# Kernel optimization log

Measured on AMD Instinct MI355X. Metric: run time of the kernel, lower is better.

Reference implementation:

```python
import jax, jax.numpy as jnp
import numpy as np

B, S, D, H = 4, 2048, 1024, 16
DK = D // H  # 64


def setup_inputs() -> dict:
    key = jax.random.key(0)
    ks = jax.random.split(key, 9)
    x = jax.random.normal(ks[0], (B, S, D), dtype=jnp.float32)
    # causal mask, broadcast over batch and heads
    attn_mask = jnp.tril(jnp.ones((S, S), dtype=jnp.int32))[None, None]
    scale = 0.02
    Wq = jax.random.normal(ks[1], (D, D), dtype=jnp.float32) * scale
    Wk = jax.random.normal(ks[2], (D, D), dtype=jnp.float32) * scale
    Wv = jax.random.normal(ks[3], (D, D), dtype=jnp.float32) * scale
    Wo = jax.random.normal(ks[4], (D, D), dtype=jnp.float32) * scale
    bq = jax.random.normal(ks[5], (D,), dtype=jnp.float32) * scale
    bk = jax.random.normal(ks[6], (D,), dtype=jnp.float32) * scale
    bv = jax.random.normal(ks[7], (D,), dtype=jnp.float32) * scale
    bo = jax.random.normal(ks[8], (D,), dtype=jnp.float32) * scale
    return {"x": x, "attn_mask": attn_mask, "Wq": Wq, "bq": bq, "Wk": Wk,
            "bk": bk, "Wv": Wv, "bv": bv, "Wo": Wo, "bo": bo}


def reference(x, attn_mask, Wq, bq, Wk, bk, Wv, bv, Wo, bo):
    b, s, d = x.shape
    # projections -> [b, h, s, dk]
    def proj(W, bias):
        return (x @ W + bias).reshape(b, s, H, DK).transpose(0, 2, 1, 3)
    q = proj(Wq, bq)
    k = proj(Wk, bk)
    v = proj(Wv, bv)
    # scores [b, h, s, s]
    scores = jnp.einsum('bhqd,bhkd->bhqk', q, k) / jnp.sqrt(jnp.float32(DK))
    scores = jnp.where(attn_mask == 0, jnp.float32(-1e9), scores)
    probs = jax.nn.softmax(scores, axis=-1)  # dropout_rate=0 -> identity
    attn_out = jnp.einsum('bhqk,bhkd->bhqd', probs, v)
    # combine heads -> [b, s, d], then output projection
    attn_out = attn_out.transpose(0, 2, 1, 3).reshape(b, s, d)
    return attn_out @ Wo + bo
```

## Files before the change

### kernel.cpp

```cpp
#include <hip/hip_runtime.h>
#include <hip/hip_bf16.h>
#include <stdint.h>

#define S_LEN 2048
#define DMODEL 1024
#define NH 16
#define DK 64
#define BATCH 4
#define KDIM 1024
#define SCQ 0.18033688f

using bf16 = __hip_bfloat16;
using bf162 = __hip_bfloat162;

typedef __bf16 v_bf16x8 __attribute__((ext_vector_type(8)));
typedef short v_s16x4 __attribute__((ext_vector_type(4)));
typedef float v_f32x4 __attribute__((ext_vector_type(4)));

union PackB4 { v_s16x4 v; bf162 h[2]; };

__device__ __forceinline__ void gll16(const void* g, void* l) {
    __builtin_amdgcn_global_load_lds(
        (__attribute__((address_space(1))) unsigned int*)g,
        (__attribute__((address_space(3))) unsigned int*)l, 16, 0, 0);
}

struct alignas(8) BF4 { bf16 a, b, c, d; };

__global__ __launch_bounds__(256) void prep(
    const float* __restrict__ x, bf16* __restrict__ xb,
    const float* __restrict__ W0, const float* __restrict__ W1,
    const float* __restrict__ W2, const float* __restrict__ W3,
    bf16* __restrict__ Wt4)
{
    const int z = blockIdx.z;
    const int t = threadIdx.x;
    if (z == 4) {
        int bid = blockIdx.y * 32 + blockIdx.x;
        size_t base4 = (size_t)bid * 2048 + t;
        #pragma unroll
        for (int j = 0; j < 8; j++) {
            size_t i4 = base4 + j * 256;
            float4 v = *(const float4*)(x + i4 * 4);
            BF4 r;
            r.a = __float2bfloat16(v.x);
            r.b = __float2bfloat16(v.y);
            r.c = __float2bfloat16(v.z);
            r.d = __float2bfloat16(v.w);
            *(BF4*)(xb + i4 * 4) = r;
        }
        return;
    }
    __shared__ float tile[32][33];
    const float* W = (z == 0) ? W0 : (z == 1) ? W1 : (z == 2) ? W2 : W3;
    bf16* Wt = Wt4 + (size_t)z * DMODEL * DMODEL;
    const float sc = (z == 0) ? SCQ : 1.0f;
    int tx = t & 31, ty = t >> 5;
    int k0 = blockIdx.x * 32, n0 = blockIdx.y * 32;
    #pragma unroll
    for (int i = 0; i < 4; i++) {
        int k = k0 + ty + 8 * i;
        tile[ty + 8 * i][tx] = W[(size_t)k * DMODEL + n0 + tx];
    }
    __syncthreads();
    #pragma unroll
    for (int i = 0; i < 4; i++) {
        int n = n0 + ty + 8 * i;
        Wt[(size_t)n * DMODEL + k0 + tx] = __float2bfloat16(tile[tx][ty + 8 * i] * sc);
    }
}

__global__ __launch_bounds__(256) void gemm_qkv(
    const bf16* __restrict__ A, const bf16* __restrict__ Wt4,
    const float* __restrict__ bq, const float* __restrict__ bk,
    const float* __restrict__ bv,
    bf16* __restrict__ Qo, bf16* __restrict__ Ko, bf16* __restrict__ Vto)
{
    __shared__ __align__(16) short lds[16384];
    const int z = blockIdx.z;
    const bf16* Bt = Wt4 + (size_t)z * DMODEL * DMODEL;
    const float* bias = (z == 0) ? bq : (z == 1) ? bk : bv;
    const float bsc = (z == 0) ? SCQ : 1.0f;

    const int t = threadIdx.x;
    const int lane = t & 63;
    const int wave = t >> 6;
    const int quad = lane >> 4;
    const int l15 = lane & 15;
    const int m0 = blockIdx.x * 128;
    const int n0 = blockIdx.y * 128;
    const int wRow = (wave >> 1) * 64;
    const int wCol = (wave & 1) * 64;

    const int r0 = t >> 2, p0 = t & 3;
    const int r1 = (t + 256) >> 2, p1 = (t + 256) & 3;

    const bf16* gA0 = A  + (size_t)(m0 + r0) * KDIM + p0 * 8;
    const bf16* gA1 = A  + (size_t)(m0 + r1) * KDIM + p1 * 8;
    const bf16* gB0 = Bt + (size_t)(n0 + r0) * KDIM + p0 * 8;
    const bf16* gB1 = Bt + (size_t)(n0 + r1) * KDIM + p1 * 8;

    v_f32x4 acc[4][4] = {};

    gll16(gA0, lds + t * 8);
    gll16(gA1, lds + t * 8 + 2048);
    gll16(gB0, lds + 4096 + t * 8);
    gll16(gB1, lds + 4096 + t * 8 + 2048);
    __syncthreads();

    int cur = 0;
    for (int k0 = 0; k0 < KDIM; k0 += 32) {
        if (k0 + 32 < KDIM) {
            short* Ad = lds + (cur ^ 1) * 8192;
            short* Bd = Ad + 4096;
            gll16(gA0 + k0 + 32, Ad + t * 8);
            gll16(gA1 + k0 + 32, Ad + t * 8 + 2048);
            gll16(gB0 + k0 + 32, Bd + t * 8);
            gll16(gB1 + k0 + 32, Bd + t * 8 + 2048);
        }
        const short* As = lds + cur * 8192;
        const short* Bs = As + 4096;
        const short* ArowBase = (z == 2) ? Bs : As;
        const short* BrowBase = (z == 2) ? As : Bs;

        v_bf16x8 af[4], bfr[4];
        #pragma unroll
        for (int mt = 0; mt < 4; mt++) {
            int r = wRow + mt * 16 + l15;
            af[mt] = *(const v_bf16x8*)(ArowBase + r * 32 + quad * 8);
        }
        #pragma unroll
        for (int nt = 0; nt < 4; nt++) {
            int r = wCol + nt * 16 + l15;
            bfr[nt] = *(const v_bf16x8*)(BrowBase + r * 32 + quad * 8);
        }
        __builtin_amdgcn_s_setprio(1);
        #pragma unroll
        for (int mt = 0; mt < 4; mt++)
            #pragma unroll
            for (int nt = 0; nt < 4; nt++)
                acc[mt][nt] = __builtin_amdgcn_mfma_f32_16x16x32_bf16(
                    af[mt], bfr[nt], acc[mt][nt], 0, 0, 0);
        __builtin_amdgcn_s_setprio(0);

        __syncthreads();
        cur ^= 1;
    }

    if (z != 2) {
        bf16* C = (z == 0) ? Qo : Ko;
        float bvv[4];
        #pragma unroll
        for (int nt = 0; nt < 4; nt++)
            bvv[nt] = bias[n0 + wCol + nt * 16 + l15] * bsc;
        #pragma unroll
        for (int mt = 0; mt < 4; mt++)
            #pragma unroll
            for (int nt = 0; nt < 4; nt++)
                #pragma unroll
                for (int r = 0; r < 4; r++) {
                    int row = m0 + wRow + mt * 16 + quad * 4 + r;
                    int col = n0 + wCol + nt * 16 + l15;
                    int b = row >> 11, s = row & (S_LEN - 1);
                    int h = col >> 6, dk = col & (DK - 1);
                    C[(((size_t)(b * NH + h)) * S_LEN + s) * DK + dk] =
                        __float2bfloat16(acc[mt][nt][r] + bvv[nt]);
                }
    } else {
        float bvv[4][4];
        #pragma unroll
        for (int mt = 0; mt < 4; mt++)
            #pragma unroll
            for (int r = 0; r < 4; r++)
                bvv[mt][r] = bias[n0 + wRow + mt * 16 + quad * 4 + r];
        #pragma unroll
        for (int mt = 0; mt < 4; mt++)
            #pragma unroll
            for (int nt = 0; nt < 4; nt++)
                #pragma unroll
                for (int r = 0; r < 4; r++) {
                    int ng = n0 + wRow + mt * 16 + quad * 4 + r;
                    int rowg = m0 + wCol + nt * 16 + l15;
                    int b = rowg >> 11, s = rowg & (S_LEN - 1);
                    int h = ng >> 6, dk = ng & (DK - 1);
                    Vto[(((size_t)(b * NH + h)) * DK + dk) * S_LEN + s] =
                        __float2bfloat16(acc[mt][nt][r] + bvv[mt][r]);
                }
    }
}

__global__ __launch_bounds__(256) void gemm_o(
    const bf16* __restrict__ A, const bf16* __restrict__ Bt,
    const float* __restrict__ bias, float* __restrict__ C)
{
    __shared__ __align__(16) short lds[16384];
    const int t = threadIdx.x;
    const int lane = t & 63;
    const int wave = t >> 6;
    const int quad = lane >> 4;
    const int l15 = lane & 15;
    const int m0 = blockIdx.x * 128;
    const int n0 = blockIdx.y * 128;
    const int wRow = (wave >> 1) * 64;
    const int wCol = (wave & 1) * 64;

    const int r0 = t >> 2, p0 = t & 3;
    const int r1 = (t + 256) >> 2, p1 = (t + 256) & 3;

    const bf16* gA0 = A  + (size_t)(m0 + r0) * KDIM + p0 * 8;
    const bf16* gA1 = A  + (size_t)(m0 + r1) * KDIM + p1 * 8;
    const bf16* gB0 = Bt + (size_t)(n0 + r0) * KDIM + p0 * 8;
    const bf16* gB1 = Bt + (size_t)(n0 + r1) * KDIM + p1 * 8;

    v_f32x4 acc[4][4] = {};

    gll16(gA0, lds + t * 8);
    gll16(gA1, lds + t * 8 + 2048);
    gll16(gB0, lds + 4096 + t * 8);
    gll16(gB1, lds + 4096 + t * 8 + 2048);
    __syncthreads();

    int cur = 0;
    for (int k0 = 0; k0 < KDIM; k0 += 32) {
        if (k0 + 32 < KDIM) {
            short* Ad = lds + (cur ^ 1) * 8192;
            short* Bd = Ad + 4096;
            gll16(gA0 + k0 + 32, Ad + t * 8);
            gll16(gA1 + k0 + 32, Ad + t * 8 + 2048);
            gll16(gB0 + k0 + 32, Bd + t * 8);
            gll16(gB1 + k0 + 32, Bd + t * 8 + 2048);
        }
        const short* As = lds + cur * 8192;
        const short* Bs = As + 4096;

        v_bf16x8 af[4], bfr[4];
        #pragma unroll
        for (int mt = 0; mt < 4; mt++) {
            int r = wRow + mt * 16 + l15;
            af[mt] = *(const v_bf16x8*)(As + r * 32 + quad * 8);
        }
        #pragma unroll
        for (int nt = 0; nt < 4; nt++) {
            int r = wCol + nt * 16 + l15;
            bfr[nt] = *(const v_bf16x8*)(Bs + r * 32 + quad * 8);
        }
        __builtin_amdgcn_s_setprio(1);
        #pragma unroll
        for (int mt = 0; mt < 4; mt++)
            #pragma unroll
            for (int nt = 0; nt < 4; nt++)
                acc[mt][nt] = __builtin_amdgcn_mfma_f32_16x16x32_bf16(
                    af[mt], bfr[nt], acc[mt][nt], 0, 0, 0);
        __builtin_amdgcn_s_setprio(0);

        __syncthreads();
        cur ^= 1;
    }

    float bvv[4];
    #pragma unroll
    for (int nt = 0; nt < 4; nt++) bvv[nt] = bias[n0 + wCol + nt * 16 + l15];

    #pragma unroll
    for (int mt = 0; mt < 4; mt++)
        #pragma unroll
        for (int nt = 0; nt < 4; nt++)
            #pragma unroll
            for (int r = 0; r < 4; r++) {
                int row = m0 + wRow + mt * 16 + quad * 4 + r;
                int col = n0 + wCol + nt * 16 + l15;
                C[(size_t)row * DMODEL + col] = acc[mt][nt][r] + bvv[nt];
            }
}

__global__ __launch_bounds__(256) void attn_mfma(
    const bf16* __restrict__ Qg, const bf16* __restrict__ Kg,
    const bf16* __restrict__ Vtg, bf16* __restrict__ Og)
{
    __shared__ __align__(16) short lds[16384];

    const int t = threadIdx.x;
    const int lane = t & 63;
    const int wave = t >> 6;
    const int quad = lane >> 4;
    const int l15 = lane & 15;
    const int bh = blockIdx.x;
    const int ybal[16] = {15, 8, 7, 0, 14, 9, 6, 1, 13, 10, 5, 2, 12, 11, 4, 3};
    const int by = blockIdx.y;
    const int yy = ybal[(by & 3) * 4 + (by >> 2)];
    const int q0 = yy * 128;
    const int ntiles = 2 * (yy + 1);

    const size_t baseK = (size_t)bh * S_LEN * DK;
    const size_t baseVt = (size_t)bh * DK * S_LEN;

    const int cr = t >> 3;
    const int cs = (t & 7) ^ (cr & 7);
    const bf16* srcK = Kg + baseK + (size_t)cr * DK + cs * 8;
    const bf16* srcV = Vtg + baseVt + (size_t)cr * S_LEN + cs * 8;

    v_bf16x8 qf[2][2];
    #pragma unroll
    for (int qt = 0; qt < 2; qt++) {
        int q = q0 + wave * 32 + qt * 16 + l15;
        #pragma unroll
        for (int kc = 0; kc < 2; kc++)
            qf[qt][kc] = *(const v_bf16x8*)(Qg + baseK + (size_t)q * DK + kc * 32 + quad * 8);
    }

    v_f32x4 oacc[2][4] = {};
    float lrun[2] = {0.f, 0.f};

    {
        short* Kd = lds;
        short* Vd = lds + 4096;
        gll16(srcK, Kd + t * 8);
        gll16(srcK + 32 * DK, Kd + t * 8 + 2048);
        gll16(srcV, Vd + t * 8);
        gll16(srcV + 32 * S_LEN, Vd + t * 8 + 2048);
    }
    __syncthreads();

    int cur = 0;
    for (int tt = 0; tt < ntiles; tt++) {
        if (tt + 1 < ntiles) {
            short* Kd = lds + (cur ^ 1) * 8192;
            short* Vd = Kd + 4096;
            const bf16* sk = srcK + (size_t)(tt + 1) * (64 * DK);
            const bf16* sv = srcV + (size_t)(tt + 1) * 64;
            gll16(sk, Kd + t * 8);
            gll16(sk + 32 * DK, Kd + t * 8 + 2048);
            gll16(sv, Vd + t * 8);
            gll16(sv + 32 * S_LEN, Vd + t * 8 + 2048);
        }
        const short* Ks = lds + cur * 8192;
        const short* Vs = Ks + 4096;

        v_f32x4 s_[4][2];
        __builtin_amdgcn_s_setprio(1);
        #pragma unroll
        for (int kt = 0; kt < 4; kt++) {
            int krow = kt * 16 + l15;
            v_bf16x8 kf0 = *(const v_bf16x8*)(Ks + krow * 64 + ((quad) ^ (krow & 7)) * 8);
            v_bf16x8 kf1 = *(const v_bf16x8*)(Ks + krow * 64 + ((4 + quad) ^ (krow & 7)) * 8);
            #pragma unroll
            for (int qt = 0; qt < 2; qt++) {
                v_f32x4 a = {};
                a = __builtin_amdgcn_mfma_f32_16x16x32_bf16(kf0, qf[qt][0], a, 0, 0, 0);
                a = __builtin_amdgcn_mfma_f32_16x16x32_bf16(kf1, qf[qt][1], a, 0, 0, 0);
                s_[kt][qt] = a;
            }
        }
        __builtin_amdgcn_s_setprio(0);

        if (tt >= ntiles - 2) {
            int kbase = (tt - (ntiles - 2)) * 64;
            #pragma unroll
            for (int kt = 0; kt < 4; kt++)
                #pragma unroll
                for (int qt = 0; qt < 2; qt++) {
                    int qq = wave * 32 + qt * 16 + l15;
                    #pragma unroll
                    for (int r = 0; r < 4; r++) {
                        int key = kbase + kt * 16 + quad * 4 + r;
                        if (key > qq) s_[kt][qt][r] = -1e30f;
                    }
                }
        }

        #pragma unroll
        for (int kt = 0; kt < 4; kt++)
            #pragma unroll
            for (int qt = 0; qt < 2; qt++) {
                float p0 = __builtin_amdgcn_exp2f(s_[kt][qt][0]);
                float p1 = __builtin_amdgcn_exp2f(s_[kt][qt][1]);
                float p2 = __builtin_amdgcn_exp2f(s_[kt][qt][2]);
                float p3 = __builtin_amdgcn_exp2f(s_[kt][qt][3]);
                s_[kt][qt][0] = p0; s_[kt][qt][1] = p1;
                s_[kt][qt][2] = p2; s_[kt][qt][3] = p3;
                lrun[qt] += (p0 + p1) + (p2 + p3);
            }

        __builtin_amdgcn_s_setprio(1);
        #pragma unroll
        for (int kt = 0; kt < 4; kt++) {
            v_s16x4 vf[4];
            #pragma unroll
            for (int dt = 0; dt < 4; dt++) {
                vf[dt] = *(const v_s16x4*)(Vs + (dt * 16 + l15) * 64 +
                                           ((kt * 2 + (quad >> 1)) ^ (l15 & 7)) * 8 +
                                           (quad & 1) * 4);
            }
            #pragma unroll
            for (int qt = 0; qt < 2; qt++) {
                PackB4 pu;
                pu.h[0] = __float22bfloat162_rn(make_float2(s_[kt][qt][0], s_[kt][qt][1]));
                pu.h[1] = __float22bfloat162_rn(make_float2(s_[kt][qt][2], s_[kt][qt][3]));
                #pragma unroll
                for (int dt = 0; dt < 4; dt++)
                    oacc[qt][dt] = __builtin_amdgcn_mfma_f32_16x16x16bf16_1k(
                        vf[dt], pu.v, oacc[qt][dt], 0, 0, 0);
            }
        }
        __builtin_amdgcn_s_setprio(0);

        __syncthreads();
        cur ^= 1;
    }

    #pragma unroll
    for (int qt = 0; qt < 2; qt++) {
        lrun[qt] += __shfl_xor(lrun[qt], 16);
        lrun[qt] += __shfl_xor(lrun[qt], 32);
    }
    #pragma unroll
    for (int qt = 0; qt < 2; qt++) {
        float inv = 1.f / lrun[qt];
        int qloc = wave * 32 + qt * 16 + l15;
        #pragma unroll
        for (int dt = 0; dt < 4; dt++) {
            PackB4 ou;
            ou.h[0] = __float22bfloat162_rn(
                make_float2(oacc[qt][dt][0] * inv, oacc[qt][dt][1] * inv));
            ou.h[1] = __float22bfloat162_rn(
                make_float2(oacc[qt][dt][2] * inv, oacc[qt][dt][3] * inv));
            *(v_s16x4*)(lds + qloc * 72 + dt * 16 + quad * 4) = ou.v;
        }
    }
    __syncthreads();
    {
        const int b = bh >> 4, h = bh & 15;
        int row = t >> 1, half = t & 1;
        size_t gbase = (((size_t)b * S_LEN + q0 + row) * NH + h) * DK + half * 32;
        #pragma unroll
        for (int j = 0; j < 4; j++)
            *(uint4*)(Og + gbase + j * 8) =
                *(const uint4*)(lds + row * 72 + half * 32 + j * 8);
    }
}

extern "C" void kernel_launch(void* const* d_in, const int* in_sizes, int n_in,
                              void* d_out, int out_size, void* d_ws, size_t ws_size,
                              hipStream_t stream) {
    const float* x  = (const float*)d_in[0];
    const float* Wq = (const float*)d_in[2];
    const float* bq = (const float*)d_in[3];
    const float* Wk = (const float*)d_in[4];
    const float* bk = (const float*)d_in[5];
    const float* Wv = (const float*)d_in[6];
    const float* bv = (const float*)d_in[7];
    const float* Wo = (const float*)d_in[8];
    const float* bo = (const float*)d_in[9];
    float* out = (float*)d_out;

    const size_t TEN = (size_t)BATCH * S_LEN * DMODEL * sizeof(bf16);
    char* ws = (char*)d_ws;
    bf16* xb  = (bf16*)ws;
    bf16* Vt  = (bf16*)(ws + TEN);
    bf16* Wt4 = (bf16*)(ws + 2 * TEN);
    bf16* Q   = (bf16*)d_out;
    bf16* Kt  = (bf16*)((char*)d_out + TEN);
    bf16* AO  = xb;

    hipLaunchKernelGGL(prep, dim3(32, 32, 5), dim3(256),
                       0, stream, x, xb, Wq, Wk, Wv, Wo, Wt4);

    hipLaunchKernelGGL(gemm_qkv, dim3(BATCH * S_LEN / 128, DMODEL / 128, 3), dim3(256),
                       0, stream, xb, Wt4, bq, bk, bv, Q, Kt, Vt);

    hipLaunchKernelGGL(attn_mfma, dim3(BATCH * NH, S_LEN / 128), dim3(256),
                       0, stream, Q, Kt, Vt, AO);

    hipLaunchKernelGGL(gemm_o, dim3(BATCH * S_LEN / 128, DMODEL / 128), dim3(256),
                       0, stream, AO, Wt4 + (size_t)3 * DMODEL * DMODEL, bo, out);
}
```

Measured before the change: 255.6 us.

## Replace syncthreads with explicit vmcnt waits and compute softmax row sums via MFMA

In both projection GEMMs, the full __syncthreads before and after each K step becomes an explicit s_waitcnt vmcnt on the async LDS loads plus a raw s_barrier, so the next tile's prefetch can stay in flight across the barrier. In the attention kernel, the per-row probability sums are now accumulated with an extra MFMA against a ones vector instead of scalar adds and cross-lane shuffles. The probabilities are packed to bf16 once and V-fragment LDS addresses are precomputed. This trades VALU and shuffle work for extra MFMA issue, and the denominator is now summed from bf16-rounded probabilities, matching the numerator's rounding.

```diff
diff --git a/kernel.cpp b/kernel.cpp
--- a/kernel.cpp
+++ b/kernel.cpp
@@ -106,7 +106,6 @@
     gll16(gA1, lds + t * 8 + 2048);
     gll16(gB0, lds + 4096 + t * 8);
     gll16(gB1, lds + 4096 + t * 8 + 2048);
-    __syncthreads();
 
     int cur = 0;
     for (int k0 = 0; k0 < KDIM; k0 += 32) {
@@ -117,7 +116,13 @@
             gll16(gA1 + k0 + 32, Ad + t * 8 + 2048);
             gll16(gB0 + k0 + 32, Bd + t * 8);
             gll16(gB1 + k0 + 32, Bd + t * 8 + 2048);
-        }
+            asm volatile("s_waitcnt vmcnt(4)" ::: "memory");
+        } else {
+            asm volatile("s_waitcnt vmcnt(0)" ::: "memory");
+        }
+        __builtin_amdgcn_sched_barrier(0);
+        __builtin_amdgcn_s_barrier();
+
         const short* As = lds + cur * 8192;
         const short* Bs = As + 4096;
         const short* ArowBase = (z == 2) ? Bs : As;
@@ -143,7 +148,9 @@
                     af[mt], bfr[nt], acc[mt][nt], 0, 0, 0);
         __builtin_amdgcn_s_setprio(0);
 
-        __syncthreads();
+        asm volatile("s_waitcnt lgkmcnt(0)" ::: "memory");
+        __builtin_amdgcn_sched_barrier(0);
+        __builtin_amdgcn_s_barrier();
         cur ^= 1;
     }
 
@@ -218,7 +225,6 @@
     gll16(gA1, lds + t * 8 + 2048);
     gll16(gB0, lds + 4096 + t * 8);
     gll16(gB1, lds + 4096 + t * 8 + 2048);
-    __syncthreads();
 
     int cur = 0;
     for (int k0 = 0; k0 < KDIM; k0 += 32) {
@@ -229,7 +235,13 @@
             gll16(gA1 + k0 + 32, Ad + t * 8 + 2048);
             gll16(gB0 + k0 + 32, Bd + t * 8);
             gll16(gB1 + k0 + 32, Bd + t * 8 + 2048);
-        }
+            asm volatile("s_waitcnt vmcnt(4)" ::: "memory");
+        } else {
+            asm volatile("s_waitcnt vmcnt(0)" ::: "memory");
+        }
+        __builtin_amdgcn_sched_barrier(0);
+        __builtin_amdgcn_s_barrier();
+
         const short* As = lds + cur * 8192;
         const short* Bs = As + 4096;
 
@@ -253,7 +265,9 @@
                     af[mt], bfr[nt], acc[mt][nt], 0, 0, 0);
         __builtin_amdgcn_s_setprio(0);
 
-        __syncthreads();
+        asm volatile("s_waitcnt lgkmcnt(0)" ::: "memory");
+        __builtin_amdgcn_sched_barrier(0);
+        __builtin_amdgcn_s_barrier();
         cur ^= 1;
     }
 
@@ -308,8 +322,19 @@
             qf[qt][kc] = *(const v_bf16x8*)(Qg + baseK + (size_t)q * DK + kc * 32 + quad * 8);
     }
 
+    int vfA[4][4];
+    #pragma unroll
+    for (int kt = 0; kt < 4; kt++)
+        #pragma unroll
+        for (int dt = 0; dt < 4; dt++)
+            vfA[kt][dt] = ((dt * 16 + l15) * 64 +
+                           ((kt * 2 + (quad >> 1)) ^ (l15 & 7)) * 8 +
+                           (quad & 1) * 4) * 2 + 8192;
+
+    const v_s16x4 ones = {(short)0x3F80, (short)0x3F80, (short)0x3F80, (short)0x3F80};
+
     v_f32x4 oacc[2][4] = {};
-    float lrun[2] = {0.f, 0.f};
+    v_f32x4 lacc[2] = {};
 
     {
         short* Kd = lds;
@@ -333,8 +358,8 @@
             gll16(sv, Vd + t * 8);
             gll16(sv + 32 * S_LEN, Vd + t * 8 + 2048);
         }
+        const int cb = cur << 14;
         const short* Ks = lds + cur * 8192;
-        const short* Vs = Ks + 4096;
 
         v_f32x4 s_[4][2];
         __builtin_amdgcn_s_setprio(1);
@@ -368,6 +393,7 @@
                 }
         }
 
+        PackB4 pk[4][2];
         #pragma unroll
         for (int kt = 0; kt < 4; kt++)
             #pragma unroll
@@ -376,9 +402,8 @@
                 float p1 = __builtin_amdgcn_exp2f(s_[kt][qt][1]);
                 float p2 = __builtin_amdgcn_exp2f(s_[kt][qt][2]);
                 float p3 = __builtin_amdgcn_exp2f(s_[kt][qt][3]);
-                s_[kt][qt][0] = p0; s_[kt][qt][1] = p1;
-                s_[kt][qt][2] = p2; s_[kt][qt][3] = p3;
-                lrun[qt] += (p0 + p1) + (p2 + p3);
+                pk[kt][qt].h[0] = __float22bfloat162_rn(make_float2(p0, p1));
+                pk[kt][qt].h[1] = __float22bfloat162_rn(make_float2(p2, p3));
             }
 
         __builtin_amdgcn_s_setprio(1);
@@ -386,20 +411,16 @@
         for (int kt = 0; kt < 4; kt++) {
             v_s16x4 vf[4];
             #pragma unroll
-            for (int dt = 0; dt < 4; dt++) {
-                vf[dt] = *(const v_s16x4*)(Vs + (dt * 16 + l15) * 64 +
-                                           ((kt * 2 + (quad >> 1)) ^ (l15 & 7)) * 8 +
-                                           (quad & 1) * 4);
-            }
+            for (int dt = 0; dt < 4; dt++)
+                vf[dt] = *(const v_s16x4*)((const char*)lds + cb + vfA[kt][dt]);
             #pragma unroll
             for (int qt = 0; qt < 2; qt++) {
-                PackB4 pu;
-                pu.h[0] = __float22bfloat162_rn(make_float2(s_[kt][qt][0], s_[kt][qt][1]));
-                pu.h[1] = __float22bfloat162_rn(make_float2(s_[kt][qt][2], s_[kt][qt][3]));
+                lacc[qt] = __builtin_amdgcn_mfma_f32_16x16x16bf16_1k(
+                    ones, pk[kt][qt].v, lacc[qt], 0, 0, 0);
                 #pragma unroll
                 for (int dt = 0; dt < 4; dt++)
                     oacc[qt][dt] = __builtin_amdgcn_mfma_f32_16x16x16bf16_1k(
-                        vf[dt], pu.v, oacc[qt][dt], 0, 0, 0);
+                        vf[dt], pk[kt][qt].v, oacc[qt][dt], 0, 0, 0);
             }
         }
         __builtin_amdgcn_s_setprio(0);
@@ -410,12 +431,7 @@
 
     #pragma unroll
     for (int qt = 0; qt < 2; qt++) {
-        lrun[qt] += __shfl_xor(lrun[qt], 16);
-        lrun[qt] += __shfl_xor(lrun[qt], 32);
-    }
-    #pragma unroll
-    for (int qt = 0; qt < 2; qt++) {
-        float inv = 1.f / lrun[qt];
+        float inv = 1.f / lacc[qt][0];
         int qloc = wave * 32 + qt * 16 + l15;
         #pragma unroll
         for (int dt = 0; dt < 4; dt++) {
```

After: 268.0 us. 1.05x slower.
